# Performance work log

Measured on AMD Instinct MI355X. Metric: run time of the kernel, lower is better.

Reference implementation:

```python
import jax, jax.numpy as jnp
import numpy as np

N_HEAD = 16
NEG_INF = -1e9


def setup_inputs() -> dict:
    key = jax.random.key(0)
    ks = jax.random.split(key, 5)
    B, T, C = 2, 2048, 1024
    scale = 1.0 / np.sqrt(C)
    return {
        "x": jax.random.normal(ks[0], (B, T, C), dtype=jnp.float32),
        "wq": jax.random.normal(ks[1], (C, C), dtype=jnp.float32) * scale,
        "bq": jnp.zeros((C,), dtype=jnp.float32),
        "wk": jax.random.normal(ks[2], (C, C), dtype=jnp.float32) * scale,
        "bk": jnp.zeros((C,), dtype=jnp.float32),
        "wv": jax.random.normal(ks[3], (C, C), dtype=jnp.float32) * scale,
        "bv": jnp.zeros((C,), dtype=jnp.float32),
        "wo": jax.random.normal(ks[4], (C, C), dtype=jnp.float32) * scale,
        "bo": jnp.zeros((C,), dtype=jnp.float32),
    }


def reference(x, wq, bq, wk, bk, wv, bv, wo, bo):
    B, T, C = x.shape
    H = N_HEAD
    d = C // H
    # linear projections, split into heads: [B, T, H, d]
    q = (x @ wq + bq).reshape(B, T, H, d)
    k = (x @ wk + bk).reshape(B, T, H, d)
    v = (x @ wv + bv).reshape(B, T, H, d)
    # scaled dot-product attention scores: [B, H, Tq, Tk]
    scores = jnp.einsum("bqhd,bkhd->bhqk", q, k) / jnp.sqrt(jnp.float32(d))
    # causal mask: triu(diagonal=1) positions are masked out
    causal = jnp.triu(jnp.ones((T, T), dtype=bool), k=1)
    scores = jnp.where(causal[None, None, :, :], NEG_INF, scores)
    attn = jax.nn.softmax(scores, axis=-1)
    # weighted values, merge heads: [B, T, C]
    out = jnp.einsum("bhqk,bkhd->bqhd", attn, v).reshape(B, T, C)
    # output projection (dropout is identity in eval / p=0)
    return out @ wo + bo
```

## Files before the change

### kernel.cpp

```cpp
#include <hip/hip_runtime.h>
#include <cstdint>
#include <type_traits>


#define TSEQ  2048
#define BATCH 2
#define CDIM  1024
#define NHEAD 16
#define DHEAD 64
#define NROWS (BATCH * TSEQ)

#define QSCALE 0.1803368801111244f

typedef unsigned short u16;
typedef u16   u16x8  __attribute__((ext_vector_type(8)));
typedef __bf16 bf16x8 __attribute__((ext_vector_type(8)));
typedef __bf16 bf16x2 __attribute__((ext_vector_type(2)));
typedef float f32x4  __attribute__((ext_vector_type(4)));

typedef const __attribute__((address_space(1))) void* gas_vp;
typedef __attribute__((address_space(3))) void* las_vp;

__device__ __forceinline__ u16 f2bf(float f) {
  return __builtin_bit_cast(u16, (__bf16)f);
}

__device__ __forceinline__ uint32_t pack2bf(float a, float b) {
  bf16x2 v;
  v[0] = (__bf16)a;
  v[1] = (__bf16)b;
  return __builtin_bit_cast(uint32_t, v);
}

__device__ __forceinline__ f32x4 mfma_bf16(u16x8 a, u16x8 b, f32x4 c) {
  return __builtin_amdgcn_mfma_f32_16x16x32_bf16(
      __builtin_bit_cast(bf16x8, a), __builtin_bit_cast(bf16x8, b), c, 0, 0, 0);
}

__device__ __forceinline__ void gload16(const u16* g, u16* l) {
  __builtin_amdgcn_global_load_lds((gas_vp)g, (las_vp)l, 16, 0, 0);
}


__global__ __launch_bounds__(256) void cast_x_kernel(const float* __restrict__ in,
                                                     u16* __restrict__ out, int n4) {
  int i = blockIdx.x * 256 + threadIdx.x;
  if (i < n4) {
    float4 v = ((const float4*)in)[i];
    ((uint2*)out)[i] = make_uint2(pack2bf(v.x, v.y), pack2bf(v.z, v.w));
  }
}

__global__ __launch_bounds__(256) void transpose_cast_kernel(
    const float* __restrict__ w0, const float* __restrict__ w1,
    const float* __restrict__ w2, const float* __restrict__ w3,
    u16* __restrict__ outQKV, u16* __restrict__ outO) {
  __shared__ float tile[32][33];
  const int m = blockIdx.z;
  const float* w = (m == 0) ? w0 : (m == 1) ? w1 : (m == 2) ? w2 : w3;
  const float scale = (m == 0) ? QSCALE : 1.0f;
  u16* out = (m < 3) ? (outQKV + (size_t)m * CDIM * CDIM) : outO;
  const int n0 = blockIdx.x * 32;
  const int k0 = blockIdx.y * 32;
  const int tx = threadIdx.x, ty = threadIdx.y;
#pragma unroll
  for (int i = 0; i < 4; ++i)
    tile[ty + i * 8][tx] = w[(size_t)(k0 + ty + i * 8) * CDIM + n0 + tx];
  __syncthreads();
#pragma unroll
  for (int i = 0; i < 4; ++i)
    out[(size_t)(n0 + ty + i * 8) * CDIM + k0 + tx] = f2bf(tile[tx][ty + i * 8] * scale);
}

__global__ __launch_bounds__(256) void bias_concat_kernel(const float* __restrict__ bq,
                                                          const float* __restrict__ bk,
                                                          const float* __restrict__ bv,
                                                          float* __restrict__ out) {
  int i = blockIdx.x * 256 + threadIdx.x;
  if (i < 3 * CDIM) {
    float v = (i < CDIM) ? bq[i] * QSCALE
            : (i < 2 * CDIM) ? bk[i - CDIM] : bv[i - 2 * CDIM];
    out[i] = v;
  }
}

__global__ __launch_bounds__(256) void vtrans_kernel(const u16* __restrict__ QKV,
                                                     u16* __restrict__ Vt) {
  __shared__ u16 tile[32][33];
  const int bh = blockIdx.z;
  const int b = bh >> 4, h = bh & 15;
  const int t0 = blockIdx.x * 32, d0 = blockIdx.y * 32;
  const int tx = threadIdx.x, ty = threadIdx.y;
#pragma unroll
  for (int i = 0; i < 4; ++i)
    tile[ty + i * 8][tx] =
        QKV[(size_t)(b * TSEQ + t0 + ty + i * 8) * (3 * CDIM) + 2 * CDIM + h * DHEAD + d0 + tx];
  __syncthreads();
#pragma unroll
  for (int i = 0; i < 4; ++i)
    Vt[(size_t)((b * NHEAD + h) * DHEAD + d0 + ty + i * 8) * TSEQ + t0 + tx] =
        tile[tx][ty + i * 8];
}


template <typename OutT>
__global__ __launch_bounds__(256) void gemm_bt_kernel(
    const u16* __restrict__ A, const u16* __restrict__ Bt,
    const float* __restrict__ bias, OutT* __restrict__ C,
    int M, int N, int K, int mblocks) {
  __shared__ u16 As[128 * 32];
  __shared__ u16 Bs[128 * 32];
  const int nwg = gridDim.x;
  const int lid = blockIdx.x;
  const int swz = (lid & 7) * (nwg >> 3) + (lid >> 3);
  const int m0 = (swz % mblocks) * 128;
  const int n0 = (swz / mblocks) * 128;

  const int t = threadIdx.x;
  const int lane = t & 63;
  const int w = t >> 6;
  const int wr = w >> 1, wc = w & 1;
  const int l15 = lane & 15;
  const int lg = lane >> 4;
  const int srow = lane >> 2;
  const int scol = (lane & 3) * 8;

  f32x4 acc[4][4];
#pragma unroll
  for (int i = 0; i < 4; ++i)
#pragma unroll
    for (int j = 0; j < 4; ++j) acc[i][j] = f32x4{0.f, 0.f, 0.f, 0.f};

  for (int k0 = 0; k0 < K; k0 += 32) {
    __syncthreads();
#pragma unroll
    for (int ci = 0; ci < 2; ++ci) {
      const int chunk = w * 2 + ci;
      const int grow = chunk * 16 + srow;
      gload16(&A[(size_t)(m0 + grow) * K + k0 + scol], &As[chunk * 512]);
      gload16(&Bt[(size_t)(n0 + grow) * K + k0 + scol], &Bs[chunk * 512]);
    }
    __syncthreads();
    u16x8 af[4], bf[4];
#pragma unroll
    for (int i = 0; i < 4; ++i)
      af[i] = *(const u16x8*)(&As[(wr * 64 + i * 16 + l15) * 32 + lg * 8]);
#pragma unroll
    for (int j = 0; j < 4; ++j)
      bf[j] = *(const u16x8*)(&Bs[(wc * 64 + j * 16 + l15) * 32 + lg * 8]);
#pragma unroll
    for (int i = 0; i < 4; ++i)
#pragma unroll
      for (int j = 0; j < 4; ++j) acc[i][j] = mfma_bf16(af[i], bf[j], acc[i][j]);
  }

#pragma unroll
  for (int j = 0; j < 4; ++j) {
    int col = n0 + wc * 64 + j * 16 + l15;
    float bv = bias[col];
#pragma unroll
    for (int i = 0; i < 4; ++i) {
#pragma unroll
      for (int r = 0; r < 4; ++r) {
        int row = m0 + wr * 64 + i * 16 + lg * 4 + r;
        float val = acc[i][j][r] + bv;
        if constexpr (std::is_same<OutT, float>::value)
          C[(size_t)row * N + col] = val;
        else
          C[(size_t)row * N + col] = f2bf(val);
      }
    }
  }
}


__global__ __launch_bounds__(512) void attn_kernel(const u16* __restrict__ QKV,
                                                   const u16* __restrict__ Vt,
                                                   u16* __restrict__ O) {
  __shared__ u16 Ks[64 * 64];
  __shared__ u16 Vs[64 * 64];
  __shared__ u16 Ps[8 * 16 * 64];

  char* KsB = (char*)Ks;
  char* VsB = (char*)Vs;

  const int t = threadIdx.x;
  const int lane = t & 63;
  const int w = t >> 6;
  const int l15 = lane & 15, lg = lane >> 4;
  const int xorv = (l15 & 7) << 4;

  const int lid = blockIdx.x;
  const int xcd = lid & 7;
  const int m = lid >> 3;
  const int bh = (m & 3) * 8 + xcd;
  const int qt = 15 - (m >> 2);
  const int b = bh >> 4, h = bh & 15;
  const int q0 = qt * 128;
  const int qrow = q0 + w * 16;
  const int nkt = (qt + 1) * 2;

  const size_t RS = 3 * CDIM;
  const u16* Qp  = QKV + (size_t)(b * TSEQ) * RS + h * DHEAD;
  const u16* Kp  = Qp + CDIM;
  const u16* Vgp = Vt + (size_t)(b * NHEAD + h) * DHEAD * TSEQ;
  char* PwB = (char*)&Ps[w * 16 * 64];

  u16x8 qf[2];
#pragma unroll
  for (int c = 0; c < 2; ++c)
    qf[c] = *(const u16x8*)(&Qp[(size_t)(qrow + l15) * RS + c * 32 + lg * 8]);

  f32x4 acc[4];
#pragma unroll
  for (int g = 0; g < 4; ++g) acc[g] = f32x4{0.f, 0.f, 0.f, 0.f};
  float m_run = -3e38f, l_run = 0.f;

  const int sr = t >> 3;
  const int sch = t & 7;
  const int swA = sr * 128 + ((sch * 16) ^ ((sr & 7) << 4));

  u16x8 kreg = *(const u16x8*)(&Kp[(size_t)sr * RS + sch * 8]);
  u16x8 vreg = *(const u16x8*)(&Vgp[(size_t)sr * TSEQ + sch * 8]);

  for (int kb = 0; kb < nkt; ++kb) {
    __syncthreads();
    *(u16x8*)(KsB + swA) = kreg;
    *(u16x8*)(VsB + swA) = vreg;
    __syncthreads();

    if (kb + 1 < nkt) {
      kreg = *(const u16x8*)(&Kp[(size_t)((kb + 1) * 64 + sr) * RS + sch * 8]);
      vreg = *(const u16x8*)(&Vgp[(size_t)sr * TSEQ + (kb + 1) * 64 + sch * 8]);
    }

    if (kb * 64 > qrow + 15) continue;

    f32x4 sfr[4];
    __builtin_amdgcn_s_setprio(1);
#pragma unroll
    for (int f = 0; f < 4; ++f) {
      const char* rowp = KsB + (f * 16 + l15) * 128;
      u16x8 k0 = *(const u16x8*)(rowp + ((lg * 16) ^ xorv));
      u16x8 k1 = *(const u16x8*)(rowp + ((64 + lg * 16) ^ xorv));
      f32x4 s = mfma_bf16(k0, qf[0], f32x4{0.f, 0.f, 0.f, 0.f});
      sfr[f] = mfma_bf16(k1, qf[1], s);
    }
    __builtin_amdgcn_s_setprio(0);

    if (kb * 64 + 63 > qrow) {
      const int q_abs = qrow + l15;
#pragma unroll
      for (int f = 0; f < 4; ++f) {
        const int kbase = kb * 64 + f * 16 + lg * 4;
#pragma unroll
        for (int r = 0; r < 4; ++r)
          if (kbase + r > q_abs) sfr[f][r] = -1e9f;
      }
    }

    float mx = sfr[0][0];
#pragma unroll
    for (int f = 0; f < 4; ++f)
#pragma unroll
      for (int r = 0; r < 4; ++r) mx = fmaxf(mx, sfr[f][r]);

    if (__any(mx > m_run + 8.f)) {
      float gm = mx;
      gm = fmaxf(gm, __shfl_xor(gm, 16));
      gm = fmaxf(gm, __shfl_xor(gm, 32));
      float mnew = fmaxf(m_run, gm);
      float fac = exp2f(m_run - mnew);
      m_run = mnew;
      l_run *= fac;
#pragma unroll
      for (int g = 0; g < 4; ++g) acc[g] *= fac;
    }

    {
      char* pb = PwB + l15 * 128;
      float ls = 0.f;
#pragma unroll
      for (int f = 0; f < 4; ++f) {
        float p0 = exp2f(sfr[f][0] - m_run);
        float p1 = exp2f(sfr[f][1] - m_run);
        float p2 = exp2f(sfr[f][2] - m_run);
        float p3 = exp2f(sfr[f][3] - m_run);
        ls += (p0 + p1) + (p2 + p3);
        const int boff = (f * 32 + lg * 8) ^ xorv;
        *(uint32_t*)(pb + boff) = pack2bf(p0, p1);
        *(uint32_t*)(pb + boff + 4) = pack2bf(p2, p3);
      }
      l_run += ls;
    }

    __builtin_amdgcn_s_setprio(1);
#pragma unroll
    for (int c = 0; c < 2; ++c) {
      const int coff = (c * 64 + lg * 16) ^ xorv;
      u16x8 pf = *(const u16x8*)(PwB + l15 * 128 + coff);
#pragma unroll
      for (int g = 0; g < 4; ++g) {
        u16x8 vf = *(const u16x8*)(VsB + (g * 16 + l15) * 128 + coff);
        acc[g] = mfma_bf16(vf, pf, acc[g]);
      }
    }
    __builtin_amdgcn_s_setprio(0);
  }

  float lt = l_run;
  lt += __shfl_xor(lt, 16);
  lt += __shfl_xor(lt, 32);
  float inv = 1.f / lt;
  {
    char* pb = PwB + l15 * 128;
#pragma unroll
    for (int g = 0; g < 4; ++g) {
      const int boff = (g * 32 + lg * 8) ^ xorv;
      *(uint32_t*)(pb + boff) = pack2bf(acc[g][0] * inv, acc[g][1] * inv);
      *(uint32_t*)(pb + boff + 4) = pack2bf(acc[g][2] * inv, acc[g][3] * inv);
    }
  }
#pragma unroll
  for (int i = 0; i < 2; ++i) {
    const int rl = i * 8 + (lane >> 3);
    const int ch = lane & 7;
    u16x8 vv = *(const u16x8*)(PwB + rl * 128 + ((ch * 16) ^ ((rl & 7) << 4)));
    *(u16x8*)(&O[(size_t)(b * TSEQ + qrow + rl) * CDIM + h * DHEAD + ch * 8]) = vv;
  }
}


extern "C" void kernel_launch(void* const* d_in, const int* in_sizes, int n_in,
                              void* d_out, int out_size, void* d_ws, size_t ws_size,
                              hipStream_t stream) {
  const float* x  = (const float*)d_in[0];
  const float* wq = (const float*)d_in[1];
  const float* bq = (const float*)d_in[2];
  const float* wk = (const float*)d_in[3];
  const float* bk = (const float*)d_in[4];
  const float* wv = (const float*)d_in[5];
  const float* bv = (const float*)d_in[6];
  const float* wo = (const float*)d_in[7];
  const float* bo = (const float*)d_in[8];
  float* out = (float*)d_out;

  char* ws = (char*)d_ws;
  u16*  xb      = (u16*)(ws);
  u16*  Vtg     = (u16*)(ws);
  u16*  wqkvT   = (u16*)(ws + (8ll << 20));
  u16*  woT     = (u16*)(ws + (14ll << 20));
  u16*  QKV     = (u16*)(ws + (16ll << 20));
  u16*  Obuf    = (u16*)(ws + (40ll << 20));
  float* biasqkv = (float*)(ws + (48ll << 20));

  cast_x_kernel<<<(NROWS * CDIM / 4 + 255) / 256, 256, 0, stream>>>(x, xb, NROWS * CDIM / 4);
  {
    dim3 g(CDIM / 32, CDIM / 32, 4), blk(32, 8);
    transpose_cast_kernel<<<g, blk, 0, stream>>>(wq, wk, wv, wo, wqkvT, woT);
  }
  bias_concat_kernel<<<12, 256, 0, stream>>>(bq, bk, bv, biasqkv);
  gemm_bt_kernel<u16><<<(NROWS / 128) * ((3 * CDIM) / 128), 256, 0, stream>>>(
      xb, wqkvT, biasqkv, QKV, NROWS, 3 * CDIM, CDIM, NROWS / 128);
  {
    dim3 g(TSEQ / 32, DHEAD / 32, BATCH * NHEAD), blk(32, 8);
    vtrans_kernel<<<g, blk, 0, stream>>>(QKV, Vtg);
  }
  attn_kernel<<<512, 512, 0, stream>>>(QKV, Vtg, Obuf);
  gemm_bt_kernel<float><<<(NROWS / 128) * (CDIM / 128), 256, 0, stream>>>(
      Obuf, woT, bo, out, NROWS, CDIM, CDIM, NROWS / 128);
}
```

Measured before the change: 133.8 us.

## Double-buffer K/V tiles in attention and widen GEMM K-step with XOR-swizzled LDS

The attention kernel now keeps two shared-memory buffers for K and V tiles. The next tile is written into the idle buffer while the current one is consumed, so each iteration needs one barrier instead of two. The GEMM kernel loads 64-wide K slices instead of 32, using XOR-swizzled LDS layout to avoid bank conflicts, which halves the number of loop iterations and barriers. Both changes increase shared memory use per block, which can lower occupancy.

```diff
diff --git a/kernel.cpp b/kernel.cpp
--- a/kernel.cpp
+++ b/kernel.cpp
@@ -108,8 +108,8 @@
     const u16* __restrict__ A, const u16* __restrict__ Bt,
     const float* __restrict__ bias, OutT* __restrict__ C,
     int M, int N, int K, int mblocks) {
-  __shared__ u16 As[128 * 32];
-  __shared__ u16 Bs[128 * 32];
+  __shared__ u16 As[128 * 64];
+  __shared__ u16 Bs[128 * 64];
   const int nwg = gridDim.x;
   const int lid = blockIdx.x;
   const int swz = (lid & 7) * (nwg >> 3) + (lid >> 3);
@@ -122,8 +122,10 @@
   const int wr = w >> 1, wc = w & 1;
   const int l15 = lane & 15;
   const int lg = lane >> 4;
-  const int srow = lane >> 2;
-  const int scol = (lane & 3) * 8;
+  const int xorv = (l15 & 7) << 4;
+
+  const int srow8 = lane >> 3;
+  const int scol_swz = ((((lane & 7) << 4) ^ (srow8 << 4)) >> 1);
 
   f32x4 acc[4][4];
 #pragma unroll
@@ -131,27 +133,32 @@
 #pragma unroll
     for (int j = 0; j < 4; ++j) acc[i][j] = f32x4{0.f, 0.f, 0.f, 0.f};
 
-  for (int k0 = 0; k0 < K; k0 += 32) {
+  for (int k0 = 0; k0 < K; k0 += 64) {
     __syncthreads();
 #pragma unroll
-    for (int ci = 0; ci < 2; ++ci) {
-      const int chunk = w * 2 + ci;
-      const int grow = chunk * 16 + srow;
-      gload16(&A[(size_t)(m0 + grow) * K + k0 + scol], &As[chunk * 512]);
-      gload16(&Bt[(size_t)(n0 + grow) * K + k0 + scol], &Bs[chunk * 512]);
+    for (int ci = 0; ci < 4; ++ci) {
+      const int c = w * 4 + ci;
+      const int grow = c * 8 + srow8;
+      gload16(&A[(size_t)(m0 + grow) * K + k0 + scol_swz], &As[c * 512]);
+      gload16(&Bt[(size_t)(n0 + grow) * K + k0 + scol_swz], &Bs[c * 512]);
     }
     __syncthreads();
-    u16x8 af[4], bf[4];
-#pragma unroll
-    for (int i = 0; i < 4; ++i)
-      af[i] = *(const u16x8*)(&As[(wr * 64 + i * 16 + l15) * 32 + lg * 8]);
-#pragma unroll
-    for (int j = 0; j < 4; ++j)
-      bf[j] = *(const u16x8*)(&Bs[(wc * 64 + j * 16 + l15) * 32 + lg * 8]);
-#pragma unroll
-    for (int i = 0; i < 4; ++i)
-#pragma unroll
-      for (int j = 0; j < 4; ++j) acc[i][j] = mfma_bf16(af[i], bf[j], acc[i][j]);
+#pragma unroll
+    for (int kk = 0; kk < 2; ++kk) {
+      u16x8 af[4], bf[4];
+#pragma unroll
+      for (int i = 0; i < 4; ++i)
+        af[i] = *(const u16x8*)((char*)As + (wr * 64 + i * 16 + l15) * 128 +
+                                ((kk * 64 + lg * 16) ^ xorv));
+#pragma unroll
+      for (int j = 0; j < 4; ++j)
+        bf[j] = *(const u16x8*)((char*)Bs + (wc * 64 + j * 16 + l15) * 128 +
+                                ((kk * 64 + lg * 16) ^ xorv));
+#pragma unroll
+      for (int i = 0; i < 4; ++i)
+#pragma unroll
+        for (int j = 0; j < 4; ++j) acc[i][j] = mfma_bf16(af[i], bf[j], acc[i][j]);
+    }
   }
 
 #pragma unroll
@@ -177,12 +184,9 @@
 __global__ __launch_bounds__(512) void attn_kernel(const u16* __restrict__ QKV,
                                                    const u16* __restrict__ Vt,
                                                    u16* __restrict__ O) {
-  __shared__ u16 Ks[64 * 64];
-  __shared__ u16 Vs[64 * 64];
+  __shared__ u16 Ks[2][64 * 64];
+  __shared__ u16 Vs[2][64 * 64];
   __shared__ u16 Ps[8 * 16 * 64];
-
-  char* KsB = (char*)Ks;
-  char* VsB = (char*)Vs;
 
   const int t = threadIdx.x;
   const int lane = t & 63;
@@ -222,90 +226,100 @@
 
   u16x8 kreg = *(const u16x8*)(&Kp[(size_t)sr * RS + sch * 8]);
   u16x8 vreg = *(const u16x8*)(&Vgp[(size_t)sr * TSEQ + sch * 8]);
+  *(u16x8*)((char*)Ks[0] + swA) = kreg;
+  *(u16x8*)((char*)Vs[0] + swA) = vreg;
+  kreg = *(const u16x8*)(&Kp[(size_t)(64 + sr) * RS + sch * 8]);
+  vreg = *(const u16x8*)(&Vgp[(size_t)sr * TSEQ + 64 + sch * 8]);
+  __syncthreads();
 
   for (int kb = 0; kb < nkt; ++kb) {
+    const int p = kb & 1;
+    char* KsB = (char*)Ks[p];
+    char* VsB = (char*)Vs[p];
+
+    if (kb + 1 < nkt) {
+      *(u16x8*)((char*)Ks[p ^ 1] + swA) = kreg;
+      *(u16x8*)((char*)Vs[p ^ 1] + swA) = vreg;
+    }
+    if (kb + 2 < nkt) {
+      kreg = *(const u16x8*)(&Kp[(size_t)((kb + 2) * 64 + sr) * RS + sch * 8]);
+      vreg = *(const u16x8*)(&Vgp[(size_t)sr * TSEQ + (kb + 2) * 64 + sch * 8]);
+    }
+
+    if (kb * 64 <= qrow + 15) {
+      f32x4 sfr[4];
+      __builtin_amdgcn_s_setprio(1);
+#pragma unroll
+      for (int f = 0; f < 4; ++f) {
+        const char* rowp = KsB + (f * 16 + l15) * 128;
+        u16x8 k0 = *(const u16x8*)(rowp + ((lg * 16) ^ xorv));
+        u16x8 k1 = *(const u16x8*)(rowp + ((64 + lg * 16) ^ xorv));
+        f32x4 s = mfma_bf16(k0, qf[0], f32x4{0.f, 0.f, 0.f, 0.f});
+        sfr[f] = mfma_bf16(k1, qf[1], s);
+      }
+      __builtin_amdgcn_s_setprio(0);
+
+      if (kb * 64 + 63 > qrow) {
+        const int q_abs = qrow + l15;
+#pragma unroll
+        for (int f = 0; f < 4; ++f) {
+          const int kbase = kb * 64 + f * 16 + lg * 4;
+#pragma unroll
+          for (int r = 0; r < 4; ++r)
+            if (kbase + r > q_abs) sfr[f][r] = -1e9f;
+        }
+      }
+
+      float mx = sfr[0][0];
+#pragma unroll
+      for (int f = 0; f < 4; ++f)
+#pragma unroll
+        for (int r = 0; r < 4; ++r) mx = fmaxf(mx, sfr[f][r]);
+
+      if (__any(mx > m_run + 8.f)) {
+        float gm = mx;
+        gm = fmaxf(gm, __shfl_xor(gm, 16));
+        gm = fmaxf(gm, __shfl_xor(gm, 32));
+        float mnew = fmaxf(m_run, gm);
+        float fac = exp2f(m_run - mnew);
+        m_run = mnew;
+        l_run *= fac;
+#pragma unroll
+        for (int g = 0; g < 4; ++g) acc[g] *= fac;
+      }
+
+      {
+        char* pb = PwB + l15 * 128;
+        float ls = 0.f;
+#pragma unroll
+        for (int f = 0; f < 4; ++f) {
+          float p0 = exp2f(sfr[f][0] - m_run);
+          float p1 = exp2f(sfr[f][1] - m_run);
+          float p2 = exp2f(sfr[f][2] - m_run);
+          float p3 = exp2f(sfr[f][3] - m_run);
+          ls += (p0 + p1) + (p2 + p3);
+          const int boff = (f * 32 + lg * 8) ^ xorv;
+          *(uint32_t*)(pb + boff) = pack2bf(p0, p1);
+          *(uint32_t*)(pb + boff + 4) = pack2bf(p2, p3);
+        }
+        l_run += ls;
+      }
+
+      __builtin_amdgcn_s_setprio(1);
+#pragma unroll
+      for (int c = 0; c < 2; ++c) {
+        const int coff = (c * 64 + lg * 16) ^ xorv;
+        u16x8 pf = *(const u16x8*)(PwB + l15 * 128 + coff);
+#pragma unroll
+        for (int g = 0; g < 4; ++g) {
+          u16x8 vf = *(const u16x8*)(VsB + (g * 16 + l15) * 128 + coff);
+          acc[g] = mfma_bf16(vf, pf, acc[g]);
+        }
+      }
+      __builtin_amdgcn_s_setprio(0);
+    }
+
     __syncthreads();
-    *(u16x8*)(KsB + swA) = kreg;
-    *(u16x8*)(VsB + swA) = vreg;
-    __syncthreads();
-
-    if (kb + 1 < nkt) {
-      kreg = *(const u16x8*)(&Kp[(size_t)((kb + 1) * 64 + sr) * RS + sch * 8]);
-      vreg = *(const u16x8*)(&Vgp[(size_t)sr * TSEQ + (kb + 1) * 64 + sch * 8]);
-    }
-
-    if (kb * 64 > qrow + 15) continue;
-
-    f32x4 sfr[4];
-    __builtin_amdgcn_s_setprio(1);
-#pragma unroll
-    for (int f = 0; f < 4; ++f) {
-      const char* rowp = KsB + (f * 16 + l15) * 128;
-      u16x8 k0 = *(const u16x8*)(rowp + ((lg * 16) ^ xorv));
-      u16x8 k1 = *(const u16x8*)(rowp + ((64 + lg * 16) ^ xorv));
-      f32x4 s = mfma_bf16(k0, qf[0], f32x4{0.f, 0.f, 0.f, 0.f});
-      sfr[f] = mfma_bf16(k1, qf[1], s);
-    }
-    __builtin_amdgcn_s_setprio(0);
-
-    if (kb * 64 + 63 > qrow) {
-      const int q_abs = qrow + l15;
-#pragma unroll
-      for (int f = 0; f < 4; ++f) {
-        const int kbase = kb * 64 + f * 16 + lg * 4;
-#pragma unroll
-        for (int r = 0; r < 4; ++r)
-          if (kbase + r > q_abs) sfr[f][r] = -1e9f;
-      }
-    }
-
-    float mx = sfr[0][0];
-#pragma unroll
-    for (int f = 0; f < 4; ++f)
-#pragma unroll
-      for (int r = 0; r < 4; ++r) mx = fmaxf(mx, sfr[f][r]);
-
-    if (__any(mx > m_run + 8.f)) {
-      float gm = mx;
-      gm = fmaxf(gm, __shfl_xor(gm, 16));
-      gm = fmaxf(gm, __shfl_xor(gm, 32));
-      float mnew = fmaxf(m_run, gm);
-      float fac = exp2f(m_run - mnew);
-      m_run = mnew;
-      l_run *= fac;
-#pragma unroll
-      for (int g = 0; g < 4; ++g) acc[g] *= fac;
-    }
-
-    {
-      char* pb = PwB + l15 * 128;
-      float ls = 0.f;
-#pragma unroll
-      for (int f = 0; f < 4; ++f) {
-        float p0 = exp2f(sfr[f][0] - m_run);
-        float p1 = exp2f(sfr[f][1] - m_run);
-        float p2 = exp2f(sfr[f][2] - m_run);
-        float p3 = exp2f(sfr[f][3] - m_run);
-        ls += (p0 + p1) + (p2 + p3);
-        const int boff = (f * 32 + lg * 8) ^ xorv;
-        *(uint32_t*)(pb + boff) = pack2bf(p0, p1);
-        *(uint32_t*)(pb + boff + 4) = pack2bf(p2, p3);
-      }
-      l_run += ls;
-    }
-
-    __builtin_amdgcn_s_setprio(1);
-#pragma unroll
-    for (int c = 0; c < 2; ++c) {
-      const int coff = (c * 64 + lg * 16) ^ xorv;
-      u16x8 pf = *(const u16x8*)(PwB + l15 * 128 + coff);
-#pragma unroll
-      for (int g = 0; g < 4; ++g) {
-        u16x8 vf = *(const u16x8*)(VsB + (g * 16 + l15) * 128 + coff);
-        acc[g] = mfma_bf16(vf, pf, acc[g]);
-      }
-    }
-    __builtin_amdgcn_s_setprio(0);
   }
 
   float lt = l_run;
```

After: 136.0 us. Within noise of the previous version (+1.6%).
